# Optimization experiments

Hardware: AMD Instinct MI355X
Metric: run time of the kernel (lower is better)

## Reference

```python
import jax, jax.numpy as jnp
import numpy as np

N = 2048            # number_of_nodes
E = 32768           # random edges (avg degree 16); self-loops added in forward
D_IN = 3            # node attrs: uncertainty, agent_presence, target
D_PAD = 5           # padded feature width (original pads [N,3] -> [N,5] with zeros)
D_H = 3             # GAT hidden / MHA embed / TransformerConv dims
L_GAT = 10          # GAT num_layers


def _seg_softmax(logits, seg, n):
    # numerically-stable softmax over incoming edges of each destination node
    m = jax.ops.segment_max(logits, seg, num_segments=n)
    e = jnp.exp(logits - m[seg])
    s = jax.ops.segment_sum(e, seg, num_segments=n)
    return e / (s[seg] + 1e-16)


def setup_inputs() -> dict:
    key = jax.random.key(0)
    ks = jax.random.split(key, 32)
    def nrm(k, shape, scale=0.3):
        return (jax.random.normal(k, shape) * scale).astype(jnp.float32)
    return {
        "x": jax.random.uniform(ks[0], (N, D_IN), dtype=jnp.float32),
        "edge_index": jax.random.randint(ks[1], (2, E), 0, N, dtype=jnp.int32),
        "mask": jax.random.uniform(ks[2], (N,), dtype=jnp.float32),
        # 10-layer GAT (heads=1): first layer 5->3, rest 3->3
        "gat_W0": nrm(ks[3], (D_PAD, D_H)),
        "gat_W": nrm(ks[4], (L_GAT - 1, D_H, D_H)),
        "gat_att_src": nrm(ks[5], (L_GAT, D_H)),
        "gat_att_dst": nrm(ks[6], (L_GAT, D_H)),
        "gat_bias": nrm(ks[7], (L_GAT, D_H)),
        # MultiheadAttention(embed_dim=3, num_heads=3, head_dim=1)
        "mha_Wq": nrm(ks[8], (D_H, D_H)), "mha_bq": nrm(ks[9], (D_H,)),
        "mha_Wk": nrm(ks[10], (D_H, D_H)), "mha_bk": nrm(ks[11], (D_H,)),
        "mha_Wv": nrm(ks[12], (D_H, D_H)), "mha_bv": nrm(ks[13], (D_H,)),
        "mha_Wo": nrm(ks[14], (D_H, D_H)), "mha_bo": nrm(ks[15], (D_H,)),
        # TransformerConv(3 -> 3, heads=1) with root-weight skip
        "tc_Wq": nrm(ks[16], (D_H, D_H)), "tc_bq": nrm(ks[17], (D_H,)),
        "tc_Wk": nrm(ks[18], (D_H, D_H)), "tc_bk": nrm(ks[19], (D_H,)),
        "tc_Wv": nrm(ks[20], (D_H, D_H)), "tc_bv": nrm(ks[21], (D_H,)),
        "tc_Wskip": nrm(ks[22], (D_H, D_H)), "tc_bskip": nrm(ks[23], (D_H,)),
        # actor MLP (per-node; MLPAggregation with index = arange(N)): 5 -> 16 -> 32 -> 1
        "mlp_W1": nrm(ks[24], (D_PAD, 16)), "mlp_b1": nrm(ks[25], (16,)),
        "mlp_W2": nrm(ks[26], (16, 32)), "mlp_b2": nrm(ks[27], (32,)),
        "mlp_W3": nrm(ks[28], (32, 1)), "mlp_b3": nrm(ks[29], (1,)),
        # critic Linear(1, 1)
        "critic_W": nrm(ks[30], (1, 1)), "critic_b": nrm(ks[31], (1,)),
    }


def reference(x, edge_index, mask, gat_W0, gat_W, gat_att_src, gat_att_dst, gat_bias,
              mha_Wq, mha_bq, mha_Wk, mha_bk, mha_Wv, mha_bv, mha_Wo, mha_bo,
              tc_Wq, tc_bq, tc_Wk, tc_bk, tc_Wv, tc_bv, tc_Wskip, tc_bskip,
              mlp_W1, mlp_b1, mlp_W2, mlp_b2, mlp_W3, mlp_b3, critic_W, critic_b):
    n = x.shape[0]
    # pad node features [N,3] -> [N,5] with zeros, as in original forward
    h = jnp.concatenate([x, jnp.zeros((n, D_PAD - x.shape[1]), x.dtype)], axis=1)
    # add self loops (add_self_loops in original)
    loop = jnp.arange(n, dtype=edge_index.dtype)
    ei = jnp.concatenate([edge_index, jnp.stack([loop, loop])], axis=1)
    src, dst = ei[0], ei[1]
    # ---- 10-layer GAT (heads=1), ReLU between layers, none after last ----
    for l in range(L_GAT):
        W = gat_W0 if l == 0 else gat_W[l - 1]
        hW = h @ W                                   # [N, 3]
        a_s = hW @ gat_att_src[l]                    # [N]
        a_d = hW @ gat_att_dst[l]                    # [N]
        e = jax.nn.leaky_relu(a_s[src] + a_d[dst], negative_slope=0.2)
        alpha = _seg_softmax(e, dst, n)              # per-destination softmax
        h = jax.ops.segment_sum(alpha[:, None] * hW[src], dst, num_segments=n) + gat_bias[l]
        if l < L_GAT - 1:
            h = jax.nn.relu(h)
    gat_x = h                                        # [N, 3]
    # ---- self multihead attention (first call: history == [gat_x]) ----
    q = (gat_x @ mha_Wq + mha_bq).T[:, :, None]      # [H, N, 1]; head_dim = 1
    k = (gat_x @ mha_Wk + mha_bk).T[:, :, None]
    v = (gat_x @ mha_Wv + mha_bv).T[:, :, None]
    scores = jnp.einsum('hnd,hmd->hnm', q, k)        # scale = head_dim**-0.5 = 1
    attn = jax.nn.softmax(scores, axis=-1)
    ctx = jnp.einsum('hnm,hmd->hnd', attn, v)        # [H, N, 1]
    res = ctx[:, :, 0].T @ mha_Wo + mha_bo           # [N, 3]
    # ---- TransformerConv(3 -> 3, heads=1) with root skip ----
    tq = res @ tc_Wq + tc_bq
    tk = res @ tc_Wk + tc_bk
    tv = res @ tc_Wv + tc_bv
    logits = (tq[dst] * tk[src]).sum(-1) / jnp.sqrt(3.0)
    alpha = _seg_softmax(logits, dst, n)
    agg = jax.ops.segment_sum(alpha[:, None] * tv[src], dst, num_segments=n)
    out = agg + res @ tc_Wskip + tc_bskip            # [N, 3]
    # pad again to 5 channels
    out5 = jnp.concatenate([out, jnp.zeros((n, D_PAD - out.shape[1]), out.dtype)], axis=1)
    # ---- actor: per-node MLP (MLPAggregation, index = arange(N) -> identity batching) ----
    h1 = jax.nn.relu(out5 @ mlp_W1 + mlp_b1)
    h2 = jax.nn.relu(h1 @ mlp_W2 + mlp_b2)
    results = h2 @ mlp_W3 + mlp_b3                   # [N, 1]
    new_results = results[:, 0] * mask               # [N]
    value = (results @ critic_W + critic_b).mean()   # scalar
    return new_results, value
```

## Files before the change

kernel.cpp:

```cpp
#include <hip/hip_runtime.h>
#include <cstdint>

#define NN   2048
#define EIN  32768
#define NB   64
#define BT   1024
#define OPB  32
#define ECAP 2048
#define UCAP 1024
#define EPT  (EIN / BT)
#define RS3  0.5773502691896258f

#define WS_FLAGS 0
#define WS_DONE  8192
#define WS_HA    8448
#define WS_HB    41216
#define WS_TKA   73984
#define WS_TKB   106752
#define WS_VPART 123136
#define WS_MEMSET_BYTES 8196

static __device__ __forceinline__ uint64_t cload64(const void* p) {
    return __hip_atomic_load((const uint64_t*)p, __ATOMIC_RELAXED, __HIP_MEMORY_SCOPE_AGENT);
}
static __device__ __forceinline__ void cstore64(void* p, uint64_t v) {
    __hip_atomic_store((uint64_t*)p, v, __ATOMIC_RELAXED, __HIP_MEMORY_SCOPE_AGENT);
}
static __device__ __forceinline__ float4 cloadf4(const float4* p) {
    union { float4 f; uint64_t u[2]; } c;
    c.u[0] = cload64(p); c.u[1] = cload64((const char*)p + 8);
    return c.f;
}
static __device__ __forceinline__ void cstoref4(float4* p, float4 v) {
    union { float4 f; uint64_t u[2]; } c; c.f = v;
    cstore64(p, c.u[0]); cstore64((char*)p + 8, c.u[1]);
}
static __device__ __forceinline__ float2 cloadf2(const float2* p) {
    union { float2 f; uint64_t u; } c; c.u = cload64(p); return c.f;
}
static __device__ __forceinline__ void cstoref2(float2* p, float2 v) {
    union { float2 f; uint64_t u; } c; c.f = v; cstore64(p, c.u);
}
static __device__ __forceinline__ float cloadf(const float* p) {
    union { float f; uint32_t u; } c;
    c.u = __hip_atomic_load((const uint32_t*)p, __ATOMIC_RELAXED, __HIP_MEMORY_SCOPE_AGENT);
    return c.f;
}
static __device__ __forceinline__ void cstoref(float* p, float v) {
    union { float f; uint32_t u; } c; c.f = v;
    __hip_atomic_store((uint32_t*)p, c.u, __ATOMIC_RELAXED, __HIP_MEMORY_SCOPE_AGENT);
}

static __device__ __forceinline__ void gbar(int* flags, int bid, int phase) {
    __syncthreads();
    if (threadIdx.x < 64) {
        if (threadIdx.x == 0) {
            asm volatile("s_waitcnt vmcnt(0)" ::: "memory");
            __hip_atomic_store(&flags[bid * 32], phase, __ATOMIC_RELAXED, __HIP_MEMORY_SCOPE_AGENT);
        }
        while (__hip_atomic_load(&flags[threadIdx.x * 32], __ATOMIC_RELAXED,
                                 __HIP_MEMORY_SCOPE_AGENT) < phase)
            __builtin_amdgcn_s_sleep(1);
    }
    __syncthreads();
}

__global__ __launch_bounds__(BT) void k_fused(
    const float* __restrict__ x, const int* __restrict__ ei,
    const float* __restrict__ maskp,
    const float* __restrict__ gW0, const float* __restrict__ gW,
    const float* __restrict__ atts, const float* __restrict__ attd,
    const float* __restrict__ gbias,
    const float* __restrict__ mWq, const float* __restrict__ mbq,
    const float* __restrict__ mWk, const float* __restrict__ mbk,
    const float* __restrict__ mWv, const float* __restrict__ mbv,
    const float* __restrict__ mWo, const float* __restrict__ mbo,
    const float* __restrict__ tWq, const float* __restrict__ tbq,
    const float* __restrict__ tWk, const float* __restrict__ tbk,
    const float* __restrict__ tWv, const float* __restrict__ tbv,
    const float* __restrict__ tWs, const float* __restrict__ tbs,
    const float* __restrict__ W1, const float* __restrict__ b1,
    const float* __restrict__ W2, const float* __restrict__ b2,
    const float* __restrict__ W3, const float* __restrict__ b3,
    const float* __restrict__ cW, const float* __restrict__ cb,
    char* __restrict__ ws, float* __restrict__ outp)
{
    __shared__ __align__(16) char pool[49152];
    __shared__ float4 hw4L[UCAP];
    __shared__ unsigned short srcs[ECAP];
    __shared__ unsigned short uniq[UCAP];
    __shared__ unsigned short mark[NN];
    __shared__ int offs[OPB + 1];
    __shared__ int cntL[OPB], curL[OPB], dloc[OPB];
    __shared__ int uniqCnt;
    __shared__ float4 ownH[OPB], tqL[OPB], skipL[OPB];
    __shared__ float ctxL[3][OPB];
    __shared__ float redf[96];
    __shared__ float resL[OPB];
    __shared__ float Mhd[6];

    int*    flags = (int*)(ws + WS_FLAGS);
    int*    done  = (int*)(ws + WS_DONE);
    float4* ha    = (float4*)(ws + WS_HA);
    float4* hb    = (float4*)(ws + WS_HB);
    float4* tka   = (float4*)(ws + WS_TKA);
    float2* tkb   = (float2*)(ws + WS_TKB);
    float*  vpart = (float*)(ws + WS_VPART);

    const int tid  = threadIdx.x;
    const int bid  = blockIdx.x;
    const int lane = tid & 63;
    const int wid  = tid >> 6;
    const int R0   = bid * OPB;

    int dcache[EPT];
    #pragma unroll
    for (int i = 0; i < EPT; ++i) dcache[i] = ei[EIN + tid + i * BT];

    if (tid < OPB) cntL[tid] = 1;
    __syncthreads();
    #pragma unroll
    for (int i = 0; i < EPT; ++i) {
        unsigned rel = (unsigned)(dcache[i] - R0);
        if (rel < OPB) atomicAdd(&cntL[rel], 1);
    }
    __syncthreads();
    if (tid < 64) {
        int c = (tid < OPB) ? cntL[tid] : 0;
        int v = c;
        #pragma unroll
        for (int d = 1; d < 32; d <<= 1) {
            int u = __shfl_up(v, d);
            if (tid >= d) v += u;
        }
        if (tid < OPB) {
            offs[tid + 1] = v;
            curL[tid] = v - c + 1;
            srcs[v - c] = (unsigned short)(R0 + tid);
        }
        if (tid == 0) { offs[0] = 0; uniqCnt = 0; }
    }
    __syncthreads();
    #pragma unroll
    for (int i = 0; i < EPT; ++i) {
        unsigned rel = (unsigned)(dcache[i] - R0);
        if (rel < OPB) {
            int p = atomicAdd(&curL[rel], 1);
            srcs[p] = (unsigned short)ei[tid + i * BT];
        }
    }
    mark[tid] = 0xFFFFu; mark[tid + BT] = 0xFFFFu;
    __syncthreads();

    const int totE = offs[OPB];
    for (int p = tid; p < totE; p += BT) {
        int s = srcs[p];
        if (mark[s] == 0xFFFFu) {
            int u = atomicAdd(&uniqCnt, 1);
            uniq[u] = (unsigned short)s;
            mark[s] = (unsigned short)u;
        }
    }
    __syncthreads();
    for (int p = tid; p < totE; p += BT) srcs[p] = mark[srcs[p]];
    if (tid < OPB) dloc[tid] = mark[R0 + tid];
    __syncthreads();
    const int UC = uniqCnt;

    for (int l = 0; l < 10; ++l) {
        float4* hprev = (l & 1) ? ha : hb;
        float4* hcur  = (l & 1) ? hb : ha;
        const float* W = l ? (gW + (l - 1) * 9) : gW0;
        float w00=W[0],w01=W[1],w02=W[2],w10=W[3],w11=W[4],w12=W[5],w20=W[6],w21=W[7],w22=W[8];
        float s0=atts[3*l],s1=atts[3*l+1],s2=atts[3*l+2];
        float d0=attd[3*l],d1=attd[3*l+1],d2=attd[3*l+2];
        float bb0=gbias[3*l],bb1=gbias[3*l+1],bb2=gbias[3*l+2];
        if (tid < UC) {
            int g = uniq[tid];
            float hx, hy, hz;
            if (l == 0) { hx = x[3*g]; hy = x[3*g+1]; hz = x[3*g+2]; }
            else { float4 t = cloadf4(&hprev[g]); hx = t.x; hy = t.y; hz = t.z; }
            float p0 = fmaf(hx, w00, fmaf(hy, w10, hz * w20));
            float p1 = fmaf(hx, w01, fmaf(hy, w11, hz * w21));
            float p2 = fmaf(hx, w02, fmaf(hy, w12, hz * w22));
            hw4L[tid] = make_float4(p0, p1, p2, fmaf(p0, s0, fmaf(p1, s1, p2 * s2)));
        }
        __syncthreads();
        {
            int j = tid >> 5, sub = tid & 31;
            int ps = offs[j], pe = offs[j + 1];
            float4 hd = hw4L[dloc[j]];
            float ad = fmaf(hd.x, d0, fmaf(hd.y, d1, hd.z * d2));
            float m = -1e30f, se = 0.f, a0 = 0.f, a1 = 0.f, a2 = 0.f;
            for (int p = ps + sub; p < pe; p += 32) {
                float4 hs = hw4L[srcs[p]];
                float lg = hs.w + ad;
                lg = (lg > 0.f) ? lg : 0.2f * lg;
                float nm = fmaxf(m, lg);
                float rr = __expf(m - nm);
                float wg = __expf(lg - nm);
                se = se*rr + wg;
                a0 = a0*rr + wg*hs.x;
                a1 = a1*rr + wg*hs.y;
                a2 = a2*rr + wg*hs.z;
                m = nm;
            }
            #pragma unroll
            for (int d = 1; d < 32; d <<= 1) {
                float m2 = __shfl_xor(m, d), se2 = __shfl_xor(se, d);
                float q0 = __shfl_xor(a0, d), q1 = __shfl_xor(a1, d), q2 = __shfl_xor(a2, d);
                float nm = fmaxf(m, m2);
                float f1 = __expf(m - nm), f2 = __expf(m2 - nm);
                se = se*f1 + se2*f2;
                a0 = a0*f1 + q0*f2; a1 = a1*f1 + q1*f2; a2 = a2*f1 + q2*f2;
                m = nm;
            }
            if (sub == 0) {
                float inv = 1.f / (se + 1e-16f);
                float o0 = a0*inv + bb0;
                float o1 = a1*inv + bb1;
                float o2 = a2*inv + bb2;
                if (l < 9) { o0 = fmaxf(o0,0.f); o1 = fmaxf(o1,0.f); o2 = fmaxf(o2,0.f); }
                cstoref4(&hcur[R0 + j], make_float4(o0, o1, o2, 0.f));
            }
        }
        gbar(flags, bid, l + 1);
    }

    {
        float* kk = (float*)pool;
        float* vv = (float*)(pool + 24576);
        float kmx[3] = {-3e38f,-3e38f,-3e38f}, kmn[3] = {3e38f,3e38f,3e38f};
        #pragma unroll
        for (int i = 0; i < 2; ++i) {
            int n = tid + i * BT;
            float4 g = cloadf4(&hb[n]);
            unsigned rel = (unsigned)(n - R0);
            if (rel < OPB) ownH[rel] = g;
            #pragma unroll
            for (int c = 0; c < 3; ++c) {
                float kv = fmaf(g.x, mWk[c], fmaf(g.y, mWk[3+c], fmaf(g.z, mWk[6+c], mbk[c])));
                float vvv= fmaf(g.x, mWv[c], fmaf(g.y, mWv[3+c], fmaf(g.z, mWv[6+c], mbv[c])));
                kk[c*NN + n] = kv; vv[c*NN + n] = vvv;
                kmx[c] = fmaxf(kmx[c], kv); kmn[c] = fminf(kmn[c], vvv == vvv ? kv : kv);
            }
        }
        #pragma unroll
        for (int c = 0; c < 3; ++c) {
            #pragma unroll
            for (int d = 1; d < 64; d <<= 1) {
                kmx[c] = fmaxf(kmx[c], __shfl_xor(kmx[c], d));
                kmn[c] = fminf(kmn[c], __shfl_xor(kmn[c], d));
            }
        }
        if (lane == 0) {
            #pragma unroll
            for (int c = 0; c < 3; ++c) {
                redf[wid*6 + c]     = kmx[c];
                redf[wid*6 + 3 + c] = kmn[c];
            }
        }
        __syncthreads();
        if (tid < 6) {
            bool ismax = tid < 3;
            float acc = ismax ? -3e38f : 3e38f;
            for (int w2 = 0; w2 < 16; ++w2) {
                float t = redf[w2*6 + tid];
                acc = ismax ? fmaxf(acc, t) : fminf(acc, t);
            }
            Mhd[tid] = acc;
        }
        __syncthreads();
        #pragma unroll
        for (int jr = 0; jr < 6; ++jr) {
            int r = wid * 6 + jr;
            int h = r >> 5, i2 = r & 31;
            float4 g = ownH[i2];
            float q = fmaf(g.x, mWq[h], fmaf(g.y, mWq[3+h], fmaf(g.z, mWq[6+h], mbq[h])));
            float M = (q >= 0.f) ? q * Mhd[h] : q * Mhd[3 + h];
            const float* kp = kk + h * NN;
            const float* vp = vv + h * NN;
            float sse = 0.f, ssv = 0.f;
            for (int mc = lane; mc < NN; mc += 64) {
                float e = __expf(fmaf(q, kp[mc], -M));
                sse += e; ssv = fmaf(e, vp[mc], ssv);
            }
            #pragma unroll
            for (int d = 32; d; d >>= 1) {
                sse += __shfl_xor(sse, d); ssv += __shfl_xor(ssv, d);
            }
            if (lane == 0) ctxL[h][i2] = ssv / sse;
        }
        __syncthreads();
        if (tid < OPB) {
            int n = R0 + tid;
            float c0 = ctxL[0][tid], c1 = ctxL[1][tid], c2 = ctxL[2][tid];
            float r0 = fmaf(c0, mWo[0], fmaf(c1, mWo[3], fmaf(c2, mWo[6], mbo[0])));
            float r1 = fmaf(c0, mWo[1], fmaf(c1, mWo[4], fmaf(c2, mWo[7], mbo[1])));
            float r2 = fmaf(c0, mWo[2], fmaf(c1, mWo[5], fmaf(c2, mWo[8], mbo[2])));
            float q0 = fmaf(r0, tWq[0], fmaf(r1, tWq[3], fmaf(r2, tWq[6], tbq[0])));
            float q1 = fmaf(r0, tWq[1], fmaf(r1, tWq[4], fmaf(r2, tWq[7], tbq[1])));
            float q2 = fmaf(r0, tWq[2], fmaf(r1, tWq[5], fmaf(r2, tWq[8], tbq[2])));
            tqL[tid] = make_float4(q0, q1, q2, 0.f);
            float k0 = fmaf(r0, tWk[0], fmaf(r1, tWk[3], fmaf(r2, tWk[6], tbk[0])));
            float k1 = fmaf(r0, tWk[1], fmaf(r1, tWk[4], fmaf(r2, tWk[7], tbk[1])));
            float k2 = fmaf(r0, tWk[2], fmaf(r1, tWk[5], fmaf(r2, tWk[8], tbk[2])));
            float v0 = fmaf(r0, tWv[0], fmaf(r1, tWv[3], fmaf(r2, tWv[6], tbv[0])));
            float v1 = fmaf(r0, tWv[1], fmaf(r1, tWv[4], fmaf(r2, tWv[7], tbv[1])));
            float v2 = fmaf(r0, tWv[2], fmaf(r1, tWv[5], fmaf(r2, tWv[8], tbv[2])));
            cstoref4(&tka[n], make_float4(k0, k1, k2, v0));
            cstoref2(&tkb[n], make_float2(v1, v2));
            float s0 = fmaf(r0, tWs[0], fmaf(r1, tWs[3], fmaf(r2, tWs[6], tbs[0])));
            float s1 = fmaf(r0, tWs[1], fmaf(r1, tWs[4], fmaf(r2, tWs[7], tbs[1])));
            float s2 = fmaf(r0, tWs[2], fmaf(r1, tWs[5], fmaf(r2, tWs[8], tbs[2])));
            skipL[tid] = make_float4(s0, s1, s2, 0.f);
        }
    }
    gbar(flags, bid, 11);

    {
        float4* sAL = (float4*)pool;
        float2* sBL = (float2*)(pool + 16384);
        if (tid < UC) {
            int g = uniq[tid];
            sAL[tid] = cloadf4(&tka[g]);
            sBL[tid] = cloadf2(&tkb[g]);
        }
        __syncthreads();
        int j = tid >> 5, sub = tid & 31;
        float4 qv = tqL[j];
        int ps = offs[j], pe = offs[j + 1];
        float m = -1e30f, se = 0.f, a0 = 0.f, a1 = 0.f, a2 = 0.f;
        for (int p = ps + sub; p < pe; p += 32) {
            int s = srcs[p];
            float4 A = sAL[s];
            float2 B = sBL[s];
            float lg = fmaf(qv.x, A.x, fmaf(qv.y, A.y, qv.z * A.z)) * RS3;
            float nm = fmaxf(m, lg);
            float rr = __expf(m - nm);
            float wg = __expf(lg - nm);
            se = se*rr + wg;
            a0 = a0*rr + wg*A.w;
            a1 = a1*rr + wg*B.x;
            a2 = a2*rr + wg*B.y;
            m = nm;
        }
        #pragma unroll
        for (int d = 1; d < 32; d <<= 1) {
            float m2 = __shfl_xor(m, d), se2 = __shfl_xor(se, d);
            float q0 = __shfl_xor(a0, d), q1 = __shfl_xor(a1, d), q2 = __shfl_xor(a2, d);
            float nm = fmaxf(m, m2);
            float f1 = __expf(m - nm), f2 = __expf(m2 - nm);
            se = se*f1 + se2*f2;
            a0 = a0*f1 + q0*f2; a1 = a1*f1 + q1*f2; a2 = a2*f1 + q2*f2;
            m = nm;
        }
        float inv = 1.f / (se + 1e-16f);
        float4 sk = skipL[j];
        float o0 = a0*inv + sk.x;
        float o1 = a1*inv + sk.y;
        float o2 = a2*inv + sk.z;
        float h1v[16];
        #pragma unroll
        for (int k = 0; k < 16; ++k)
            h1v[k] = fmaxf(fmaf(o0, W1[k], fmaf(o1, W1[16+k], fmaf(o2, W1[32+k], b1[k]))), 0.f);
        float t = b2[sub];
        #pragma unroll
        for (int k = 0; k < 16; ++k) t = fmaf(h1v[k], W2[k*32 + sub], t);
        float racc = fmaxf(t, 0.f) * W3[sub];
        #pragma unroll
        for (int d = 1; d < 32; d <<= 1) racc += __shfl_xor(racc, d);
        float resv = racc + b3[0];
        if (sub == 0) {
            int n = R0 + j;
            outp[n] = resv * maskp[n];
            resL[j] = resv;
        }
        __syncthreads();
        if (tid == 0) {
            float s = 0.f;
            for (int u = 0; u < OPB; ++u) s += resL[u];
            cstoref(&vpart[bid], s);
            asm volatile("s_waitcnt vmcnt(0)" ::: "memory");
            int ticket = __hip_atomic_fetch_add(done, 1, __ATOMIC_RELAXED, __HIP_MEMORY_SCOPE_AGENT);
            if (ticket == NB - 1) {
                float tsum = 0.f;
                for (int b = 0; b < NB; ++b) tsum += cloadf(&vpart[b]);
                outp[NN] = fmaf(cW[0], tsum * (1.f / (float)NN), cb[0]);
            }
        }
    }
}

extern "C" void kernel_launch(void* const* d_in, const int* in_sizes, int n_in,
                              void* d_out, int out_size, void* d_ws, size_t ws_size,
                              hipStream_t stream)
{
    const float* x    = (const float*)d_in[0];
    const int*   ei   = (const int*)  d_in[1];
    const float* mask = (const float*)d_in[2];
    const float* gW0  = (const float*)d_in[3];
    const float* gW   = (const float*)d_in[4];
    const float* atts = (const float*)d_in[5];
    const float* attd = (const float*)d_in[6];
    const float* gbias= (const float*)d_in[7];
    const float* mWq = (const float*)d_in[8];  const float* mbq = (const float*)d_in[9];
    const float* mWk = (const float*)d_in[10]; const float* mbk = (const float*)d_in[11];
    const float* mWv = (const float*)d_in[12]; const float* mbv = (const float*)d_in[13];
    const float* mWo = (const float*)d_in[14]; const float* mbo = (const float*)d_in[15];
    const float* tWq = (const float*)d_in[16]; const float* tbq = (const float*)d_in[17];
    const float* tWk = (const float*)d_in[18]; const float* tbk = (const float*)d_in[19];
    const float* tWv = (const float*)d_in[20]; const float* tbv = (const float*)d_in[21];
    const float* tWs = (const float*)d_in[22]; const float* tbs = (const float*)d_in[23];
    const float* W1  = (const float*)d_in[24]; const float* b1  = (const float*)d_in[25];
    const float* W2  = (const float*)d_in[26]; const float* b2  = (const float*)d_in[27];
    const float* W3  = (const float*)d_in[28]; const float* b3  = (const float*)d_in[29];
    const float* cW  = (const float*)d_in[30]; const float* cb  = (const float*)d_in[31];

    hipMemsetAsync(d_ws, 0, WS_MEMSET_BYTES, stream);

    k_fused<<<NB, BT, 0, stream>>>(x, ei, mask, gW0, gW, atts, attd, gbias,
                                   mWq, mbq, mWk, mbk, mWv, mbv, mWo, mbo,
                                   tWq, tbq, tWk, tbk, tWv, tbv, tWs, tbs,
                                   W1, b1, W2, b2, W3, b3, cW, cb,
                                   (char*)d_ws, (float*)d_out);
}
```

Before: 78.73 us.

## Replace grid barriers with per-element sentinel polling and two-pass segment softmax

```diff
diff --git a/kernel.cpp b/kernel.cpp
--- a/kernel.cpp
+++ b/kernel.cpp
@@ -10,59 +10,57 @@
 #define UCAP 1024
 #define EPT  (EIN / BT)
 #define RS3  0.5773502691896258f
-
-#define WS_FLAGS 0
-#define WS_DONE  8192
-#define WS_HA    8448
-#define WS_HB    41216
-#define WS_TKA   73984
-#define WS_TKB   106752
-#define WS_VPART 123136
-#define WS_MEMSET_BYTES 8196
+#define SENT 0xFFFFFFFFu
+
+#define WS_TICKET 0
+#define WS_H      128
+#define WS_TKA    (WS_H + 10*NN*16)
+#define WS_TKB    (WS_TKA + NN*16)
+#define WS_VPART  (WS_TKB + NN*8)
+#define WS_END    (WS_VPART + 256)
 
 static __device__ __forceinline__ uint64_t cload64(const void* p) {
     return __hip_atomic_load((const uint64_t*)p, __ATOMIC_RELAXED, __HIP_MEMORY_SCOPE_AGENT);
 }
 static __device__ __forceinline__ void cstore64(void* p, uint64_t v) {
     __hip_atomic_store((uint64_t*)p, v, __ATOMIC_RELAXED, __HIP_MEMORY_SCOPE_AGENT);
-}
-static __device__ __forceinline__ float4 cloadf4(const float4* p) {
-    union { float4 f; uint64_t u[2]; } c;
-    c.u[0] = cload64(p); c.u[1] = cload64((const char*)p + 8);
-    return c.f;
 }
 static __device__ __forceinline__ void cstoref4(float4* p, float4 v) {
     union { float4 f; uint64_t u[2]; } c; c.f = v;
     cstore64(p, c.u[0]); cstore64((char*)p + 8, c.u[1]);
 }
-static __device__ __forceinline__ float2 cloadf2(const float2* p) {
-    union { float2 f; uint64_t u; } c; c.u = cload64(p); return c.f;
-}
 static __device__ __forceinline__ void cstoref2(float2* p, float2 v) {
     union { float2 f; uint64_t u; } c; c.f = v; cstore64(p, c.u);
-}
-static __device__ __forceinline__ float cloadf(const float* p) {
-    union { float f; uint32_t u; } c;
-    c.u = __hip_atomic_load((const uint32_t*)p, __ATOMIC_RELAXED, __HIP_MEMORY_SCOPE_AGENT);
-    return c.f;
 }
 static __device__ __forceinline__ void cstoref(float* p, float v) {
     union { float f; uint32_t u; } c; c.f = v;
     __hip_atomic_store((uint32_t*)p, c.u, __ATOMIC_RELAXED, __HIP_MEMORY_SCOPE_AGENT);
 }
-
-static __device__ __forceinline__ void gbar(int* flags, int bid, int phase) {
-    __syncthreads();
-    if (threadIdx.x < 64) {
-        if (threadIdx.x == 0) {
-            asm volatile("s_waitcnt vmcnt(0)" ::: "memory");
-            __hip_atomic_store(&flags[bid * 32], phase, __ATOMIC_RELAXED, __HIP_MEMORY_SCOPE_AGENT);
-        }
-        while (__hip_atomic_load(&flags[threadIdx.x * 32], __ATOMIC_RELAXED,
-                                 __HIP_MEMORY_SCOPE_AGENT) < phase)
-            __builtin_amdgcn_s_sleep(1);
-    }
-    __syncthreads();
+static __device__ __forceinline__ float4 pollf4(const float4* p) {
+    uint64_t a = cload64(p);
+    uint64_t b = cload64((const char*)p + 8);
+    while ((uint32_t)a == SENT || (uint32_t)b == SENT) {
+        __builtin_amdgcn_s_sleep(1);
+        a = cload64(p);
+        b = cload64((const char*)p + 8);
+    }
+    union { uint64_t u[2]; float4 f; } c; c.u[0] = a; c.u[1] = b;
+    return c.f;
+}
+static __device__ __forceinline__ float2 pollf2(const float2* p) {
+    uint64_t a = cload64(p);
+    while ((uint32_t)a == SENT) { __builtin_amdgcn_s_sleep(1); a = cload64(p); }
+    union { uint64_t u; float2 f; } c; c.u = a;
+    return c.f;
+}
+static __device__ __forceinline__ float pollf(const float* p) {
+    uint32_t a = __hip_atomic_load((const uint32_t*)p, __ATOMIC_RELAXED, __HIP_MEMORY_SCOPE_AGENT);
+    while (a == SENT) {
+        __builtin_amdgcn_s_sleep(1);
+        a = __hip_atomic_load((const uint32_t*)p, __ATOMIC_RELAXED, __HIP_MEMORY_SCOPE_AGENT);
+    }
+    union { uint32_t u; float f; } c; c.u = a;
+    return c.f;
 }
 
 __global__ __launch_bounds__(BT) void k_fused(
@@ -99,13 +97,11 @@
     __shared__ float resL[OPB];
     __shared__ float Mhd[6];
 
-    int*    flags = (int*)(ws + WS_FLAGS);
-    int*    done  = (int*)(ws + WS_DONE);
-    float4* ha    = (float4*)(ws + WS_HA);
-    float4* hb    = (float4*)(ws + WS_HB);
-    float4* tka   = (float4*)(ws + WS_TKA);
-    float2* tkb   = (float2*)(ws + WS_TKB);
-    float*  vpart = (float*)(ws + WS_VPART);
+    int*    ticket = (int*)(ws + WS_TICKET);
+    float4* hbase  = (float4*)(ws + WS_H);
+    float4* tka    = (float4*)(ws + WS_TKA);
+    float2* tkb    = (float2*)(ws + WS_TKB);
+    float*  vpart  = (float*)(ws + WS_VPART);
 
     const int tid  = threadIdx.x;
     const int bid  = blockIdx.x;
@@ -168,8 +164,8 @@
     const int UC = uniqCnt;
 
     for (int l = 0; l < 10; ++l) {
-        float4* hprev = (l & 1) ? ha : hb;
-        float4* hcur  = (l & 1) ? hb : ha;
+        const float4* hprev = hbase + (l - 1) * NN;
+        float4*       hnext = hbase + l * NN;
         const float* W = l ? (gW + (l - 1) * 9) : gW0;
         float w00=W[0],w01=W[1],w02=W[2],w10=W[3],w11=W[4],w12=W[5],w20=W[6],w21=W[7],w22=W[8];
         float s0=atts[3*l],s1=atts[3*l+1],s2=atts[3*l+2];
@@ -179,7 +175,7 @@
             int g = uniq[tid];
             float hx, hy, hz;
             if (l == 0) { hx = x[3*g]; hy = x[3*g+1]; hz = x[3*g+2]; }
-            else { float4 t = cloadf4(&hprev[g]); hx = t.x; hy = t.y; hz = t.z; }
+            else { float4 t = pollf4(&hprev[g]); hx = t.x; hy = t.y; hz = t.z; }
             float p0 = fmaf(hx, w00, fmaf(hy, w10, hz * w20));
             float p1 = fmaf(hx, w01, fmaf(hy, w11, hz * w21));
             float p2 = fmaf(hx, w02, fmaf(hy, w12, hz * w22));
@@ -191,29 +187,31 @@
             int ps = offs[j], pe = offs[j + 1];
             float4 hd = hw4L[dloc[j]];
             float ad = fmaf(hd.x, d0, fmaf(hd.y, d1, hd.z * d2));
-            float m = -1e30f, se = 0.f, a0 = 0.f, a1 = 0.f, a2 = 0.f;
+            float m = -1e30f;
+            for (int p = ps + sub; p < pe; p += 32) {
+                float lg = hw4L[srcs[p]].w + ad;
+                lg = (lg > 0.f) ? lg : 0.2f * lg;
+                m = fmaxf(m, lg);
+            }
+            #pragma unroll
+            for (int d = 1; d < 32; d <<= 1) m = fmaxf(m, __shfl_xor(m, d));
+            float se = 0.f, a0 = 0.f, a1 = 0.f, a2 = 0.f;
             for (int p = ps + sub; p < pe; p += 32) {
                 float4 hs = hw4L[srcs[p]];
                 float lg = hs.w + ad;
                 lg = (lg > 0.f) ? lg : 0.2f * lg;
-                float nm = fmaxf(m, lg);
-                float rr = __expf(m - nm);
-                float wg = __expf(lg - nm);
-                se = se*rr + wg;
-                a0 = a0*rr + wg*hs.x;
-                a1 = a1*rr + wg*hs.y;
-                a2 = a2*rr + wg*hs.z;
-                m = nm;
+                float e = __expf(lg - m);
+                se += e;
+                a0 = fmaf(e, hs.x, a0);
+                a1 = fmaf(e, hs.y, a1);
+                a2 = fmaf(e, hs.z, a2);
             }
             #pragma unroll
             for (int d = 1; d < 32; d <<= 1) {
-                float m2 = __shfl_xor(m, d), se2 = __shfl_xor(se, d);
-                float q0 = __shfl_xor(a0, d), q1 = __shfl_xor(a1, d), q2 = __shfl_xor(a2, d);
-                float nm = fmaxf(m, m2);
-                float f1 = __expf(m - nm), f2 = __expf(m2 - nm);
-                se = se*f1 + se2*f2;
-                a0 = a0*f1 + q0*f2; a1 = a1*f1 + q1*f2; a2 = a2*f1 + q2*f2;
-                m = nm;
+                se += __shfl_xor(se, d);
+                a0 += __shfl_xor(a0, d);
+                a1 += __shfl_xor(a1, d);
+                a2 += __shfl_xor(a2, d);
             }
             if (sub == 0) {
                 float inv = 1.f / (se + 1e-16f);
@@ -221,20 +219,21 @@
                 float o1 = a1*inv + bb1;
                 float o2 = a2*inv + bb2;
                 if (l < 9) { o0 = fmaxf(o0,0.f); o1 = fmaxf(o1,0.f); o2 = fmaxf(o2,0.f); }
-                cstoref4(&hcur[R0 + j], make_float4(o0, o1, o2, 0.f));
-            }
-        }
-        gbar(flags, bid, l + 1);
+                cstoref4(&hnext[R0 + j], make_float4(o0, o1, o2, 0.f));
+            }
+        }
+        __syncthreads();
     }
 
     {
+        const float4* hf = hbase + 9 * NN;
         float* kk = (float*)pool;
         float* vv = (float*)(pool + 24576);
         float kmx[3] = {-3e38f,-3e38f,-3e38f}, kmn[3] = {3e38f,3e38f,3e38f};
         #pragma unroll
         for (int i = 0; i < 2; ++i) {
             int n = tid + i * BT;
-            float4 g = cloadf4(&hb[n]);
+            float4 g = pollf4(&hf[n]);
             unsigned rel = (unsigned)(n - R0);
             if (rel < OPB) ownH[rel] = g;
             #pragma unroll
@@ -242,7 +241,7 @@
                 float kv = fmaf(g.x, mWk[c], fmaf(g.y, mWk[3+c], fmaf(g.z, mWk[6+c], mbk[c])));
                 float vvv= fmaf(g.x, mWv[c], fmaf(g.y, mWv[3+c], fmaf(g.z, mWv[6+c], mbv[c])));
                 kk[c*NN + n] = kv; vv[c*NN + n] = vvv;
-                kmx[c] = fmaxf(kmx[c], kv); kmn[c] = fminf(kmn[c], vvv == vvv ? kv : kv);
+                kmx[c] = fmaxf(kmx[c], kv); kmn[c] = fminf(kmn[c], kv);
             }
         }
         #pragma unroll
@@ -316,44 +315,45 @@
             skipL[tid] = make_float4(s0, s1, s2, 0.f);
         }
     }
-    gbar(flags, bid, 11);
 
     {
         float4* sAL = (float4*)pool;
         float2* sBL = (float2*)(pool + 16384);
         if (tid < UC) {
             int g = uniq[tid];
-            sAL[tid] = cloadf4(&tka[g]);
-            sBL[tid] = cloadf2(&tkb[g]);
+            sAL[tid] = pollf4(&tka[g]);
+            sBL[tid] = pollf2(&tkb[g]);
         }
         __syncthreads();
         int j = tid >> 5, sub = tid & 31;
         float4 qv = tqL[j];
         int ps = offs[j], pe = offs[j + 1];
-        float m = -1e30f, se = 0.f, a0 = 0.f, a1 = 0.f, a2 = 0.f;
+        float m = -1e30f;
+        for (int p = ps + sub; p < pe; p += 32) {
+            float4 A = sAL[srcs[p]];
+            float lg = fmaf(qv.x, A.x, fmaf(qv.y, A.y, qv.z * A.z)) * RS3;
+            m = fmaxf(m, lg);
+        }
+        #pragma unroll
+        for (int d = 1; d < 32; d <<= 1) m = fmaxf(m, __shfl_xor(m, d));
+        float se = 0.f, a0 = 0.f, a1 = 0.f, a2 = 0.f;
         for (int p = ps + sub; p < pe; p += 32) {
             int s = srcs[p];
             float4 A = sAL[s];
             float2 B = sBL[s];
             float lg = fmaf(qv.x, A.x, fmaf(qv.y, A.y, qv.z * A.z)) * RS3;
-            float nm = fmaxf(m, lg);
-            float rr = __expf(m - nm);
-            float wg = __expf(lg - nm);
-            se = se*rr + wg;
-            a0 = a0*rr + wg*A.w;
-            a1 = a1*rr + wg*B.x;
-            a2 = a2*rr + wg*B.y;
-            m = nm;
+            float e = __expf(lg - m);
+            se += e;
+            a0 = fmaf(e, A.w, a0);
+            a1 = fmaf(e, B.x, a1);
+            a2 = fmaf(e, B.y, a2);
         }
         #pragma unroll
         for (int d = 1; d < 32; d <<= 1) {
-            float m2 = __shfl_xor(m, d), se2 = __shfl_xor(se, d);
-            float q0 = __shfl_xor(a0, d), q1 = __shfl_xor(a1, d), q2 = __shfl_xor(a2, d);
-            float nm = fmaxf(m, m2);
-            float f1 = __expf(m - nm), f2 = __expf(m2 - nm);
-            se = se*f1 + se2*f2;
-            a0 = a0*f1 + q0*f2; a1 = a1*f1 + q1*f2; a2 = a2*f1 + q2*f2;
-            m = nm;
+            se += __shfl_xor(se, d);
+            a0 += __shfl_xor(a0, d);
+            a1 += __shfl_xor(a1, d);
+            a2 += __shfl_xor(a2, d);
         }
         float inv = 1.f / (se + 1e-16f);
         float4 sk = skipL[j];
@@ -381,11 +381,10 @@
             float s = 0.f;
             for (int u = 0; u < OPB; ++u) s += resL[u];
             cstoref(&vpart[bid], s);
-            asm volatile("s_waitcnt vmcnt(0)" ::: "memory");
-            int ticket = __hip_atomic_fetch_add(done, 1, __ATOMIC_RELAXED, __HIP_MEMORY_SCOPE_AGENT);
-            if (ticket == NB - 1) {
+            int tk = __hip_atomic_fetch_add(ticket, 1, __ATOMIC_RELAXED, __HIP_MEMORY_SCOPE_AGENT);
+            if (tk == NB - 1) {
                 float tsum = 0.f;
-                for (int b = 0; b < NB; ++b) tsum += cloadf(&vpart[b]);
+                for (int b = 0; b < NB; ++b) tsum += pollf(&vpart[b]);
                 outp[NN] = fmaf(cW[0], tsum * (1.f / (float)NN), cb[0]);
             }
         }
@@ -417,7 +416,8 @@
     const float* W3  = (const float*)d_in[28]; const float* b3  = (const float*)d_in[29];
     const float* cW  = (const float*)d_in[30]; const float* cb  = (const float*)d_in[31];
 
-    hipMemsetAsync(d_ws, 0, WS_MEMSET_BYTES, stream);
+    hipMemsetAsync(d_ws, 0, 128, stream);
+    hipMemsetAsync((char*)d_ws + WS_H, 0xFF, WS_END - WS_H, stream);
 
     k_fused<<<NB, BT, 0, stream>>>(x, ei, mask, gW0, gW, atts, attd, gbias,
                                    mWq, mbq, mWk, mbk, mWv, mbv, mWo, mbo,
```

Result: slower. 80.86 us (+2.7%).
